# Kernel tuning notes

Hardware: AMD Instinct MI355X
Metric: run time of the kernel (lower is better)

## Reference

```python
import jax, jax.numpy as jnp
import numpy as np

INV_SQRT_4PI = 0.28209479177387814  # 1/sqrt(4*pi)

def sh_l(r, l):
    """Real spherical harmonics of unit vectors r [..., 3], e3nn order,
    'integral' normalization (e3nn o3.spherical_harmonics default)."""
    x, y, z = r[..., 0], r[..., 1], r[..., 2]
    if l == 0:
        return jnp.full(r.shape[:-1] + (1,), INV_SQRT_4PI, r.dtype)
    if l == 1:
        return 0.4886025119029199 * r  # sqrt(3/(4pi)) * (x, y, z)
    s15 = 3.872983346207417 * INV_SQRT_4PI   # sqrt(15)/sqrt(4pi)
    s5 = 2.23606797749979 * INV_SQRT_4PI     # sqrt(5)/sqrt(4pi)
    return jnp.stack([
        s15 * x * z,
        s15 * x * y,
        s5 * (y * y - 0.5 * (x * x + z * z)),
        s15 * y * z,
        0.5 * s15 * (z * z - x * x),
    ], axis=-1)

def layer_norm(x, g, b, eps=1e-5):
    mu = jnp.mean(x, axis=-1, keepdims=True)
    var = jnp.mean((x - mu) ** 2, axis=-1, keepdims=True)
    return (x - mu) * jax.lax.rsqrt(var + eps) * g + b

def setup_inputs() -> dict:
    key = jax.random.key(0)
    N, C, L = 1024, 128, 3  # nodes, sphere_channels, lmax+1
    ks = jax.random.split(key, 12)
    s = 0.02
    return {
        "x_emb": jax.random.normal(ks[0], (N, 9, C), jnp.float32),
        "pos": jax.random.normal(ks[1], (N, 3), jnp.float32) * 3.0,
        "q_w": jax.random.normal(ks[2], (C, C), jnp.float32) * s,
        "q_b": jnp.zeros((C,), jnp.float32),
        "k_w": jax.random.normal(ks[3], (C, C), jnp.float32) * s,
        "k_b": jnp.zeros((C,), jnp.float32),
        "v_w": jax.random.normal(ks[4], (L, C, C), jnp.float32) * s,
        "v_b0": jnp.zeros((C,), jnp.float32),
        "out_w": jax.random.normal(ks[5], (L, C, C), jnp.float32) * s,
        "ln_g": jnp.ones((L, C), jnp.float32),
        "ln_b": jnp.zeros((L, C), jnp.float32),
        "batch": jnp.sort(jax.random.randint(ks[6], (N,), 0, 16)).astype(jnp.int64),
    }

def reference(x_emb, pos, q_w, q_b, k_w, k_b, v_w, v_b0, out_w, ln_g, ln_b, batch):
    N, _, C = x_emb.shape
    H = 8
    D = C // H
    degs = (1, 3, 5)  # 2l+1 for l = 0, 1, 2

    # pairwise unit displacements  [N, N, 3]
    diff = pos[:, None, :] - pos[None, :, :]
    dist = jnp.maximum(jnp.linalg.norm(diff, axis=-1, keepdims=True), 1e-8)
    r_hat = diff / dist

    same = batch[:, None] == batch[None, :]           # [N, N]
    valid = same & ~jnp.eye(N, dtype=bool)

    # per-degree features: split x_emb[:, 9, C] into [1, 3, 5]
    feats = [x_emb[:, 0:1], x_emb[:, 1:4], x_emb[:, 4:9]]

    # HTR invariant pairwise score  [N, N, C]
    score = jnp.zeros((N, N, C), x_emb.dtype)
    for l, f in enumerate(feats):
        sh = sh_l(r_hat, l)                           # [N, N, 2l+1]
        score = score + jnp.einsum('imc,ijm->ijc', f, sh) / degs[l]
    score = score * valid[..., None].astype(score.dtype)

    q = (score.mean(axis=1) @ q_w.T + q_b).reshape(N, H, D)
    k = (score.mean(axis=0) @ k_w.T + k_b).reshape(N, H, D)

    attn = jnp.einsum('ihd,jhd->hij', q, k) * (D ** -0.5)
    attn = jnp.where(same[None], attn, -jnp.inf)
    attn = jnp.nan_to_num(jax.nn.softmax(attn, axis=-1))

    outs = []
    for l, f in enumerate(feats):
        m = degs[l]
        v = f @ v_w[l].T
        if l == 0:
            v = v + v_b0
        v = v.reshape(N, m, H, D)
        o = jnp.einsum('hij,jmhd->imhd', attn, v).reshape(N, m, C)
        o = o @ out_w[l].T
        outs.append(layer_norm(f + o, ln_g[l], ln_b[l]))
    return jnp.concatenate(outs, axis=1)
```

## Files before the change

kernel.cpp:

```cpp
#include <hip/hip_runtime.h>
#include <hip/hip_bf16.h>
#include <math.h>

#define NN 1024

typedef __attribute__((ext_vector_type(8))) short bf16x8;
typedef __attribute__((ext_vector_type(4))) float f32x4;

__device__ __forceinline__ float wave_sum(float v) {
#pragma unroll
  for (int off = 32; off > 0; off >>= 1) v += __shfl_down(v, off);
  return v;
}
__device__ __forceinline__ float wave_max(float v) {
#pragma unroll
  for (int off = 32; off > 0; off >>= 1) v = fmaxf(v, __shfl_down(v, off));
  return v;
}
__device__ __forceinline__ short f2bf(float x) {
  __hip_bfloat16 b = __float2bfloat16(x);
  return *(short*)&b;
}

#define SH_C0 0.28209479177387814f
#define SH_C1 0.4886025119029199f
#define SH_S15 1.0925484305920792f
#define SH_S5 0.6307831305050401f

__global__ __launch_bounds__(256) void htr_geom(
    const float* __restrict__ qw, const float* __restrict__ kw,
    const float* __restrict__ vw, const float* __restrict__ ow,
    const float* __restrict__ x_emb, const float* __restrict__ pos,
    const int* __restrict__ batch, const float* __restrict__ k_b,
    short* __restrict__ wbf, short* __restrict__ x_bf,
    short* __restrict__ fkT, short* __restrict__ Wsh,
    short* __restrict__ rowm_bf, float* __restrict__ khbuf) {
  const int b = blockIdx.x;
  const int tid = threadIdx.x;
  __shared__ short tile[128][36];
  __shared__ float red[4][9];
  __shared__ float sm[9];

  if (b < 8) {
    const float* src;
    if (b == 0) src = qw;
    else if (b == 1) src = kw;
    else if (b < 5) src = vw + (b - 2) * 16384;
    else src = ow + (b - 5) * 16384;
    short* dst = wbf + b * 16384;
    for (int idx = tid; idx < 16384; idx += 256) dst[idx] = f2bf(src[idx]);
  } else if (b < 1160) {
    int base = (b - 8) * 1024 + tid * 4;
    float4 v = *(const float4*)(x_emb + base);
    *(short4*)(x_bf + base) = make_short4(f2bf(v.x), f2bf(v.y), f2bf(v.z), f2bf(v.w));
  } else if (b < 1448) {
    const int sub = b - 1160;
    const int i0 = (sub & 31) * 32;
    const int m = sub >> 5;
    const int w = tid >> 6, lane = tid & 63;
    const int q = lane >> 4, l15 = lane & 15;
    const int isub = (w & 1) * 16;
    const int cbase = (w >> 1) * 64;
    bf16x8 a[4];
#pragma unroll
    for (int ks = 0; ks < 4; ++ks) {
      const float* ap = x_emb + ((i0 + isub + l15) * 9 + m) * 128 + ks * 32 + q * 8;
      bf16x8 av;
#pragma unroll
      for (int e = 0; e < 8; ++e) av[e] = f2bf(ap[e]);
      a[ks] = av;
    }
#pragma unroll
    for (int t = 0; t < 4; ++t) {
      f32x4 acc = (f32x4){0.f, 0.f, 0.f, 0.f};
#pragma unroll
      for (int ks = 0; ks < 4; ++ks) {
        const float* bp = kw + (cbase + t * 16 + l15) * 128 + ks * 32 + q * 8;
        bf16x8 bv;
#pragma unroll
        for (int e = 0; e < 8; ++e) bv[e] = f2bf(bp[e]);
        acc = __builtin_amdgcn_mfma_f32_16x16x32_bf16(a[ks], bv, acc, 0, 0, 0);
      }
#pragma unroll
      for (int r = 0; r < 4; ++r)
        tile[cbase + t * 16 + l15][isub + q * 4 + r] = f2bf(acc[r]);
    }
    __syncthreads();
    const int cc = tid >> 1, seg = tid & 1;
    short* dst = fkT + cc * 9216 + m * 1024 + i0 + seg * 16;
#pragma unroll
    for (int e = 0; e < 16; e += 2)
      *(short2*)(dst + e) = *(const short2*)(&tile[cc][seg * 16 + e]);
  } else if (b < 2472) {
    const int j = b - 1448;
    const float pjx = pos[j * 3 + 0], pjy = pos[j * 3 + 1], pjz = pos[j * 3 + 2];
    const int bj = batch[j];
    short* wrow = Wsh + j * 9216;
    for (int i = tid; i < 1024; i += 256) {
      float dx = pos[i * 3 + 0] - pjx;
      float dy = pos[i * 3 + 1] - pjy;
      float dz = pos[i * 3 + 2] - pjz;
      bool ok = (i != j) && (batch[i] == bj);
      float okf = ok ? 1.f : 0.f;
      float d2 = dx * dx + dy * dy + dz * dz;
      float inv = okf / fmaxf(sqrtf(d2), 1e-8f);
      float x = dx * inv, y = dy * inv, z = dz * inv;
      wrow[0 * 1024 + i] = f2bf(SH_C0 * okf);
      wrow[1 * 1024 + i] = f2bf((SH_C1 * (1.f / 3.f)) * x);
      wrow[2 * 1024 + i] = f2bf((SH_C1 * (1.f / 3.f)) * y);
      wrow[3 * 1024 + i] = f2bf((SH_C1 * (1.f / 3.f)) * z);
      wrow[4 * 1024 + i] = f2bf((SH_S15 * 0.2f) * x * z);
      wrow[5 * 1024 + i] = f2bf((SH_S15 * 0.2f) * x * y);
      wrow[6 * 1024 + i] = f2bf((SH_S5 * 0.2f) * (y * y - 0.5f * (x * x + z * z)));
      wrow[7 * 1024 + i] = f2bf((SH_S15 * 0.2f) * y * z);
      wrow[8 * 1024 + i] = f2bf((0.5f * SH_S15 * 0.2f) * (z * z - x * x));
    }
  } else if (b < 3496) {
    const int i = b - 2472;
    const float px = pos[i * 3 + 0], py = pos[i * 3 + 1], pz = pos[i * 3 + 2];
    const int bi = batch[i];
    float s[9];
#pragma unroll
    for (int m = 0; m < 9; ++m) s[m] = 0.f;
    for (int j = tid; j < NN; j += 256) {
      if (j == i) continue;
      if (batch[j] != bi) continue;
      float dx = px - pos[j * 3 + 0];
      float dy = py - pos[j * 3 + 1];
      float dz = pz - pos[j * 3 + 2];
      float d2 = dx * dx + dy * dy + dz * dz;
      float inv = 1.0f / fmaxf(sqrtf(d2), 1e-8f);
      float x = dx * inv, y = dy * inv, z = dz * inv;
      s[0] += 1.0f;
      s[1] += x; s[2] += y; s[3] += z;
      s[4] += x * z; s[5] += x * y;
      s[6] += y * y - 0.5f * (x * x + z * z);
      s[7] += y * z;
      s[8] += z * z - x * x;
    }
    const int wave = tid >> 6, lane = tid & 63;
#pragma unroll
    for (int m = 0; m < 9; ++m) {
      float v = wave_sum(s[m]);
      if (lane == 0) red[wave][m] = v;
    }
    __syncthreads();
    if (tid < 9) {
      float v = red[0][tid] + red[1][tid] + red[2][tid] + red[3][tid];
      float scl = SH_S15 * 0.2f;
      if (tid == 0) scl = SH_C0;
      else if (tid < 4) scl = SH_C1 * (1.f / 3.f);
      else if (tid == 6) scl = SH_S5 * 0.2f;
      else if (tid == 8) scl = 0.5f * SH_S15 * 0.2f;
      sm[tid] = v * scl * (1.0f / 1024.0f);
    }
    __syncthreads();
    if (tid < 128) {
      float acc = 0.f;
#pragma unroll
      for (int m = 0; m < 9; ++m)
        acc = fmaf(sm[m], x_emb[(i * 9 + m) * 128 + tid], acc);
      rowm_bf[i * 128 + tid] = f2bf(acc);
    }
  } else {
    const int base = (b - 3496) * 32768;
    for (int u = tid; u < 32768; u += 256) {
      const int idx = base + u;
      khbuf[idx] = k_b[((idx >> 14) << 4) | (idx & 15)];
    }
  }
}

__global__ __launch_bounds__(256) void htr_mid(
    const short* __restrict__ Wsh, const short* __restrict__ fkT,
    const short* __restrict__ rowm_bf, const short* __restrict__ x_bf,
    const short* __restrict__ wbf, const float* __restrict__ q_b,
    const float* __restrict__ v_b0, float* __restrict__ khbuf,
    float* __restrict__ qbuf, short* __restrict__ vbT) {
  const int b = blockIdx.x;
  const int tid = threadIdx.x;
  const int w = tid >> 6, lane = tid & 63;
  const int q = lane >> 4, l15 = lane & 15;
  __shared__ short bt[32][584];

  if (b < 256) {
    const int jb = (b & 15) * 64;
    const int ks = b >> 4;
    const int j = jb + w * 16 + l15;
    const short* ap = Wsh + j * 9216 + ks * 576 + q * 8;
    bf16x8 A[18];
#pragma unroll
    for (int s = 0; s < 18; ++s) A[s] = *(const bf16x8*)(ap + s * 32);

    f32x4 acc[8];
#pragma unroll
    for (int t = 0; t < 8; ++t) acc[t] = (f32x4){0.f, 0.f, 0.f, 0.f};

    for (int tc = 0; tc < 4; ++tc) {
      __syncthreads();
#pragma unroll
      for (int it = 0; it < 9; ++it) {
        int idx = tid + it * 256;
        int c = idx / 72;
        int g = idx - c * 72;
        *(bf16x8*)(&bt[c][g * 8]) =
            *(const bf16x8*)(fkT + (tc * 32 + c) * 9216 + ks * 576 + g * 8);
      }
      __syncthreads();
#pragma unroll
      for (int tl = 0; tl < 2; ++tl) {
        const int t = tc * 2 + tl;
        const short* brow = &bt[tl * 16 + l15][q * 8];
#pragma unroll
        for (int s = 0; s < 18; ++s) {
          bf16x8 bv = *(const bf16x8*)(brow + s * 32);
          acc[t] = __builtin_amdgcn_mfma_f32_16x16x32_bf16(A[s], bv, acc[t], 0, 0, 0);
        }
      }
    }
#pragma unroll
    for (int t = 0; t < 8; ++t)
#pragma unroll
      for (int r = 0; r < 4; ++r)
        atomicAdd(&khbuf[(t * 1024 + jb + w * 16 + q * 4 + r) * 16 + l15],
                  acc[t][r] * (1.0f / 1024.0f));
  } else if (b < 272) {
    const int ibase = ((b - 256) * 4 + w) * 16;
    const short* ap = rowm_bf + (ibase + l15) * 128 + q * 8;
    const short* bp = wbf + l15 * 128 + q * 8;
    bf16x8 a[4];
#pragma unroll
    for (int ks = 0; ks < 4; ++ks) a[ks] = *(const bf16x8*)(ap + ks * 32);
    f32x4 acc[8];
#pragma unroll
    for (int t = 0; t < 8; ++t) {
      acc[t] = (f32x4){0.f, 0.f, 0.f, 0.f};
      const short* btp = bp + t * 2048;
#pragma unroll
      for (int ks = 0; ks < 4; ++ks) {
        bf16x8 bv = *(const bf16x8*)(btp + ks * 32);
        acc[t] = __builtin_amdgcn_mfma_f32_16x16x32_bf16(a[ks], bv, acc[t], 0, 0, 0);
      }
    }
#pragma unroll
    for (int t = 0; t < 8; ++t) {
      float bo = q_b[t * 16 + l15];
#pragma unroll
      for (int r = 0; r < 4; ++r)
        qbuf[(ibase + q * 4 + r) * 128 + t * 16 + l15] = acc[t][r] + bo;
    }
  } else {
    const int u = (b - 272) * 4 + w;
    const int m = u >> 6;
    const int ibase = (u & 63) * 16;
    const int l = (m == 0) ? 0 : ((m < 4) ? 1 : 2);
    const short* ap = x_bf + ((ibase + l15) * 9 + m) * 128 + q * 8;
    const short* bp = wbf + (2 + l) * 16384 + l15 * 128 + q * 8;
    bf16x8 a[4];
#pragma unroll
    for (int ks = 0; ks < 4; ++ks) a[ks] = *(const bf16x8*)(ap + ks * 32);
    f32x4 acc[8];
#pragma unroll
    for (int t = 0; t < 8; ++t) {
      acc[t] = (f32x4){0.f, 0.f, 0.f, 0.f};
      const short* btp = bp + t * 2048;
#pragma unroll
      for (int ks = 0; ks < 4; ++ks) {
        bf16x8 bv = *(const bf16x8*)(btp + ks * 32);
        acc[t] = __builtin_amdgcn_mfma_f32_16x16x32_bf16(a[ks], bv, acc[t], 0, 0, 0);
      }
    }
#pragma unroll
    for (int t = 0; t < 8; ++t) {
      float bias = (m == 0) ? v_b0[t * 16 + l15] : 0.f;
#pragma unroll
      for (int r = 0; r < 4; ++r)
        vbT[(t * 144 + m * 16 + l15) * 1024 + ibase + q * 4 + r] =
            f2bf(acc[t][r] + bias);
    }
  }
}

template <int NT0, int NT>
__device__ __forceinline__ void apply_phase(
    const short* P, const short* __restrict__ vbT,
    short* __restrict__ obuf_bf, int ibase, int h, int lane) {
  const int q = lane >> 4, l15 = lane & 15;
  const int xs = (l15 & 7) << 3;
  const short* pr = P + l15 * 1024;
  const short* bp = vbT + (h * 144 + l15) * 1024 + q * 8;
  f32x4 acc[NT];
#pragma unroll
  for (int t = 0; t < NT; ++t) acc[t] = (f32x4){0.f, 0.f, 0.f, 0.f};
  bf16x8 a = *(const bf16x8*)(pr + ((q * 8) ^ xs));
  bf16x8 b[NT];
#pragma unroll
  for (int t = 0; t < NT; ++t) b[t] = *(const bf16x8*)(bp + (NT0 + t) * 16384);
  for (int ks = 1; ks < 32; ++ks) {
    const int off = ks * 32;
    bf16x8 an = *(const bf16x8*)(pr + ((off + q * 8) ^ xs));
    bf16x8 bn[NT];
#pragma unroll
    for (int t = 0; t < NT; ++t)
      bn[t] = *(const bf16x8*)(bp + (NT0 + t) * 16384 + off);
#pragma unroll
    for (int t = 0; t < NT; ++t)
      acc[t] = __builtin_amdgcn_mfma_f32_16x16x32_bf16(a, b[t], acc[t], 0, 0, 0);
    a = an;
#pragma unroll
    for (int t = 0; t < NT; ++t) b[t] = bn[t];
  }
#pragma unroll
  for (int t = 0; t < NT; ++t)
    acc[t] = __builtin_amdgcn_mfma_f32_16x16x32_bf16(a, b[t], acc[t], 0, 0, 0);
#pragma unroll
  for (int t = 0; t < NT; ++t)
#pragma unroll
    for (int r = 0; r < 4; ++r)
      obuf_bf[((ibase + q * 4 + r) * 9 + NT0 + t) * 128 + h * 16 + l15] =
          f2bf(acc[t][r]);
}

__global__ __launch_bounds__(256) void htr_attn_apply(
    const float* __restrict__ qbuf, const float* __restrict__ khbuf,
    const int* __restrict__ batch, const short* __restrict__ vbT,
    short* __restrict__ obuf_bf) {
  const int ibase = blockIdx.x * 16;
  const int h = blockIdx.y;
  const int tid = threadIdx.x;
  const int w = tid >> 6;
  const int lane = tid & 63;
  __shared__ short P[16 * 1024];

  const int r0 = ibase + w * 4;
  float qr[4][16];
  int bi[4];
#pragma unroll
  for (int r = 0; r < 4; ++r) {
    bi[r] = batch[r0 + r];
    const float* qp = qbuf + (r0 + r) * 128 + h * 16;
#pragma unroll
    for (int d = 0; d < 16; ++d) qr[r][d] = qp[d] * 0.25f;
  }
  float s[4][16];
#pragma unroll
  for (int jt = 0; jt < 16; ++jt) {
    const int j = jt * 64 + lane;
    const int bj = batch[j];
    const float4* kp = (const float4*)(khbuf + (h * 1024 + j) * 16);
    float4 k0 = kp[0], k1 = kp[1], k2 = kp[2], k3 = kp[3];
#pragma unroll
    for (int r = 0; r < 4; ++r) {
      float d = 0.f;
      d = fmaf(qr[r][0], k0.x, d);  d = fmaf(qr[r][1], k0.y, d);
      d = fmaf(qr[r][2], k0.z, d);  d = fmaf(qr[r][3], k0.w, d);
      d = fmaf(qr[r][4], k1.x, d);  d = fmaf(qr[r][5], k1.y, d);
      d = fmaf(qr[r][6], k1.z, d);  d = fmaf(qr[r][7], k1.w, d);
      d = fmaf(qr[r][8], k2.x, d);  d = fmaf(qr[r][9], k2.y, d);
      d = fmaf(qr[r][10], k2.z, d); d = fmaf(qr[r][11], k2.w, d);
      d = fmaf(qr[r][12], k3.x, d); d = fmaf(qr[r][13], k3.y, d);
      d = fmaf(qr[r][14], k3.z, d); d = fmaf(qr[r][15], k3.w, d);
      s[r][jt] = (bj == bi[r]) ? d : -INFINITY;
    }
  }
#pragma unroll
  for (int r = 0; r < 4; ++r) {
    float mx = s[r][0];
#pragma unroll
    for (int jt = 1; jt < 16; ++jt) mx = fmaxf(mx, s[r][jt]);
    mx = wave_max(mx);
    mx = __shfl(mx, 0);
    float t = 0.f;
#pragma unroll
    for (int jt = 0; jt < 16; ++jt) {
      s[r][jt] = expf(s[r][jt] - mx);
      t += s[r][jt];
    }
    t = wave_sum(t);
    t = __shfl(t, 0);
    const float inv = 1.0f / t;
    const int row = w * 4 + r;
    const int xs = (row & 7) << 3;
    short* pw = P + row * 1024;
#pragma unroll
    for (int jt = 0; jt < 16; ++jt) {
      const int j = jt * 64 + lane;
      pw[j ^ xs] = f2bf(s[r][jt] * inv);
    }
  }
  __syncthreads();

  if (w == 0)      apply_phase<0, 3>(P, vbT, obuf_bf, ibase, h, lane);
  else if (w == 1) apply_phase<3, 2>(P, vbT, obuf_bf, ibase, h, lane);
  else if (w == 2) apply_phase<5, 2>(P, vbT, obuf_bf, ibase, h, lane);
  else             apply_phase<7, 2>(P, vbT, obuf_bf, ibase, h, lane);
}

__global__ __launch_bounds__(64) void htr_outln_mfma(
    const short* __restrict__ obuf_bf, const float* __restrict__ x_emb,
    const short* __restrict__ wbf, const float* __restrict__ ln_g,
    const float* __restrict__ ln_b, float* __restrict__ out) {
  const int ibase = blockIdx.x * 16;
  const int m = blockIdx.y;
  const int l = (m == 0) ? 0 : ((m < 4) ? 1 : 2);
  const int lane = threadIdx.x;
  const int q = lane >> 4, l15 = lane & 15;
  const short* ap = obuf_bf + ((ibase + l15) * 9 + m) * 128 + q * 8;
  const short* bp = wbf + (5 + l) * 16384 + l15 * 128 + q * 8;
  bf16x8 a[4];
#pragma unroll
  for (int ks = 0; ks < 4; ++ks) a[ks] = *(const bf16x8*)(ap + ks * 32);
  f32x4 acc[8];
#pragma unroll
  for (int t = 0; t < 8; ++t) {
    acc[t] = (f32x4){0.f, 0.f, 0.f, 0.f};
    const short* bt = bp + t * 2048;
#pragma unroll
    for (int ks = 0; ks < 4; ++ks) {
      bf16x8 b = *(const bf16x8*)(bt + ks * 32);
      acc[t] = __builtin_amdgcn_mfma_f32_16x16x32_bf16(a[ks], b, acc[t], 0, 0, 0);
    }
  }
  float g[8], bb[8];
#pragma unroll
  for (int t = 0; t < 8; ++t) {
    g[t] = ln_g[l * 128 + t * 16 + l15];
    bb[t] = ln_b[l * 128 + t * 16 + l15];
  }
#pragma unroll
  for (int r = 0; r < 4; ++r) {
    const int i = ibase + q * 4 + r;
    const float* xr = x_emb + (i * 9 + m) * 128;
    float v[8];
    float sv = 0.f, sq = 0.f;
#pragma unroll
    for (int t = 0; t < 8; ++t) {
      v[t] = acc[t][r] + xr[t * 16 + l15];
      sv += v[t];
      sq += v[t] * v[t];
    }
#pragma unroll
    for (int off = 1; off < 16; off <<= 1) {
      sv += __shfl_xor(sv, off);
      sq += __shfl_xor(sq, off);
    }
    float mu = sv * (1.f / 128.f);
    float var = sq * (1.f / 128.f) - mu * mu;
    float rs = rsqrtf(var + 1e-5f);
    float* orow = out + (i * 9 + m) * 128;
#pragma unroll
    for (int t = 0; t < 8; ++t)
      orow[t * 16 + l15] = (v[t] - mu) * rs * g[t] + bb[t];
  }
}

extern "C" void kernel_launch(void* const* d_in, const int* in_sizes, int n_in,
                              void* d_out, int out_size, void* d_ws, size_t ws_size,
                              hipStream_t stream) {
  (void)in_sizes; (void)n_in; (void)out_size; (void)ws_size;
  const float* x_emb = (const float*)d_in[0];
  const float* pos   = (const float*)d_in[1];
  const float* q_w   = (const float*)d_in[2];
  const float* q_b   = (const float*)d_in[3];
  const float* k_w   = (const float*)d_in[4];
  const float* k_b   = (const float*)d_in[5];
  const float* v_w   = (const float*)d_in[6];
  const float* v_b0  = (const float*)d_in[7];
  const float* out_w = (const float*)d_in[8];
  const float* ln_g  = (const float*)d_in[9];
  const float* ln_b  = (const float*)d_in[10];
  const int*   batch = (const int*)d_in[11];
  float* out = (float*)d_out;

  float* ws = (float*)d_ws;
  short* rowm_bf = (short*)(ws + 0);
  float* qbuf    = ws + 65536;
  float* khbuf   = ws + 196608;
  short* wbf     = (short*)(ws + 327680);
  short* x_bf    = (short*)(ws + 393216);
  short* vbT     = (short*)(ws + 983040);
  short* obuf_bf = (short*)(ws + 1572864);
  short* Wsh     = (short*)(ws + 6356992);
  short* fkT     = (short*)(ws + 11075584);

  htr_geom<<<3500, 256, 0, stream>>>(q_w, k_w, v_w, out_w, x_emb, pos, batch,
                                     k_b, wbf, x_bf, fkT, Wsh, rowm_bf, khbuf);
  htr_mid<<<416, 256, 0, stream>>>(Wsh, fkT, rowm_bf, x_bf, wbf, q_b, v_b0,
                                   khbuf, qbuf, vbT);
  htr_attn_apply<<<dim3(64, 8), 256, 0, stream>>>(qbuf, khbuf, batch, vbT,
                                                  obuf_bf);
  htr_outln_mfma<<<dim3(64, 9), 64, 0, stream>>>(obuf_bf, x_emb, wbf, ln_g,
                                                 ln_b, out);
}
```

Measured before the change: 152.6 us.

## Compute spherical-harmonic weights in registers inside mid GEMM instead of materializing Wsh

Removes the geometry pass that wrote a 1024x9216 bf16 spherical-harmonic matrix to global memory. The mid kernel now loads positions and batch ids for a 64x64 node tile into shared memory and builds its MFMA A-fragments directly in registers. The fkT loads are re-indexed so the reduction is split by i-block rather than the old k-slice layout. This avoids about 19 MB of global writes and reads in exchange for recomputing square roots and divides inside the GEMM blocks.

```diff
diff --git a/kernel.cpp b/kernel.cpp
--- a/kernel.cpp
+++ b/kernel.cpp
@@ -33,8 +33,8 @@
     const float* __restrict__ x_emb, const float* __restrict__ pos,
     const int* __restrict__ batch, const float* __restrict__ k_b,
     short* __restrict__ wbf, short* __restrict__ x_bf,
-    short* __restrict__ fkT, short* __restrict__ Wsh,
-    short* __restrict__ rowm_bf, float* __restrict__ khbuf) {
+    short* __restrict__ fkT, short* __restrict__ rowm_bf,
+    float* __restrict__ khbuf) {
   const int b = blockIdx.x;
   const int tid = threadIdx.x;
   __shared__ short tile[128][36];
@@ -92,31 +92,7 @@
     for (int e = 0; e < 16; e += 2)
       *(short2*)(dst + e) = *(const short2*)(&tile[cc][seg * 16 + e]);
   } else if (b < 2472) {
-    const int j = b - 1448;
-    const float pjx = pos[j * 3 + 0], pjy = pos[j * 3 + 1], pjz = pos[j * 3 + 2];
-    const int bj = batch[j];
-    short* wrow = Wsh + j * 9216;
-    for (int i = tid; i < 1024; i += 256) {
-      float dx = pos[i * 3 + 0] - pjx;
-      float dy = pos[i * 3 + 1] - pjy;
-      float dz = pos[i * 3 + 2] - pjz;
-      bool ok = (i != j) && (batch[i] == bj);
-      float okf = ok ? 1.f : 0.f;
-      float d2 = dx * dx + dy * dy + dz * dz;
-      float inv = okf / fmaxf(sqrtf(d2), 1e-8f);
-      float x = dx * inv, y = dy * inv, z = dz * inv;
-      wrow[0 * 1024 + i] = f2bf(SH_C0 * okf);
-      wrow[1 * 1024 + i] = f2bf((SH_C1 * (1.f / 3.f)) * x);
-      wrow[2 * 1024 + i] = f2bf((SH_C1 * (1.f / 3.f)) * y);
-      wrow[3 * 1024 + i] = f2bf((SH_C1 * (1.f / 3.f)) * z);
-      wrow[4 * 1024 + i] = f2bf((SH_S15 * 0.2f) * x * z);
-      wrow[5 * 1024 + i] = f2bf((SH_S15 * 0.2f) * x * y);
-      wrow[6 * 1024 + i] = f2bf((SH_S5 * 0.2f) * (y * y - 0.5f * (x * x + z * z)));
-      wrow[7 * 1024 + i] = f2bf((SH_S15 * 0.2f) * y * z);
-      wrow[8 * 1024 + i] = f2bf((0.5f * SH_S15 * 0.2f) * (z * z - x * x));
-    }
-  } else if (b < 3496) {
-    const int i = b - 2472;
+    const int i = b - 1448;
     const float px = pos[i * 3 + 0], py = pos[i * 3 + 1], pz = pos[i * 3 + 2];
     const int bi = batch[i];
     float s[9];
@@ -163,7 +139,7 @@
       rowm_bf[i * 128 + tid] = f2bf(acc);
     }
   } else {
-    const int base = (b - 3496) * 32768;
+    const int base = (b - 2472) * 32768;
     for (int u = tid; u < 32768; u += 256) {
       const int idx = base + u;
       khbuf[idx] = k_b[((idx >> 14) << 4) | (idx & 15)];
@@ -172,25 +148,72 @@
 }
 
 __global__ __launch_bounds__(256) void htr_mid(
-    const short* __restrict__ Wsh, const short* __restrict__ fkT,
-    const short* __restrict__ rowm_bf, const short* __restrict__ x_bf,
-    const short* __restrict__ wbf, const float* __restrict__ q_b,
-    const float* __restrict__ v_b0, float* __restrict__ khbuf,
-    float* __restrict__ qbuf, short* __restrict__ vbT) {
+    const float* __restrict__ pos, const int* __restrict__ batch,
+    const short* __restrict__ fkT, const short* __restrict__ rowm_bf,
+    const short* __restrict__ x_bf, const short* __restrict__ wbf,
+    const float* __restrict__ q_b, const float* __restrict__ v_b0,
+    float* __restrict__ khbuf, float* __restrict__ qbuf,
+    short* __restrict__ vbT) {
   const int b = blockIdx.x;
   const int tid = threadIdx.x;
   const int w = tid >> 6, lane = tid & 63;
   const int q = lane >> 4, l15 = lane & 15;
   __shared__ short bt[32][584];
+  __shared__ float4 pj_s[64], pi_s[64];
 
   if (b < 256) {
     const int jb = (b & 15) * 64;
-    const int ks = b >> 4;
-    const int j = jb + w * 16 + l15;
-    const short* ap = Wsh + j * 9216 + ks * 576 + q * 8;
+    const int ib = (b >> 4) * 64;
+    if (tid < 64)
+      pj_s[tid] = make_float4(pos[(jb + tid) * 3 + 0], pos[(jb + tid) * 3 + 1],
+                              pos[(jb + tid) * 3 + 2],
+                              __int_as_float(batch[jb + tid]));
+    else if (tid < 128) {
+      const int u = tid - 64;
+      pi_s[u] = make_float4(pos[(ib + u) * 3 + 0], pos[(ib + u) * 3 + 1],
+                            pos[(ib + u) * 3 + 2],
+                            __int_as_float(batch[ib + u]));
+    }
+    __syncthreads();
+
+    const int jl = w * 16 + l15;
+    const int j = jb + jl;
+    const float4 pj = pj_s[jl];
+    const int bj = __float_as_int(pj.w);
+
     bf16x8 A[18];
-#pragma unroll
-    for (int s = 0; s < 18; ++s) A[s] = *(const bf16x8*)(ap + s * 32);
+    {
+#pragma unroll
+      for (int half = 0; half < 2; ++half) {
+        float gx[8], gy[8], gz[8], go[8];
+#pragma unroll
+        for (int e = 0; e < 8; ++e) {
+          const int il = half * 32 + q * 8 + e;
+          const float4 pi = pi_s[il];
+          const bool ok = ((ib + il) != j) && (__float_as_int(pi.w) == bj);
+          const float okf = ok ? 1.f : 0.f;
+          const float dx = pi.x - pj.x;
+          const float dy = pi.y - pj.y;
+          const float dz = pi.z - pj.z;
+          const float d2 = dx * dx + dy * dy + dz * dz;
+          const float inv = okf / fmaxf(sqrtf(d2), 1e-8f);
+          gx[e] = dx * inv; gy[e] = dy * inv; gz[e] = dz * inv; go[e] = okf;
+        }
+#pragma unroll
+        for (int e = 0; e < 8; ++e) {
+          const float x = gx[e], y = gy[e], z = gz[e], okf = go[e];
+          A[0 + half][e] = f2bf(SH_C0 * okf);
+          A[2 + half][e] = f2bf((SH_C1 * (1.f / 3.f)) * x);
+          A[4 + half][e] = f2bf((SH_C1 * (1.f / 3.f)) * y);
+          A[6 + half][e] = f2bf((SH_C1 * (1.f / 3.f)) * z);
+          A[8 + half][e] = f2bf((SH_S15 * 0.2f) * x * z);
+          A[10 + half][e] = f2bf((SH_S15 * 0.2f) * x * y);
+          A[12 + half][e] = f2bf((SH_S5 * 0.2f) * (y * y - 0.5f * (x * x + z * z)));
+          A[14 + half][e] = f2bf((SH_S15 * 0.2f) * y * z);
+          A[16 + half][e] = f2bf((0.5f * SH_S15 * 0.2f) * (z * z - x * x));
+        }
+      }
+    }
 
     f32x4 acc[8];
 #pragma unroll
@@ -204,7 +227,8 @@
         int c = idx / 72;
         int g = idx - c * 72;
         *(bf16x8*)(&bt[c][g * 8]) =
-            *(const bf16x8*)(fkT + (tc * 32 + c) * 9216 + ks * 576 + g * 8);
+            *(const bf16x8*)(fkT + (tc * 32 + c) * 9216 + (g >> 3) * 1024 + ib +
+                             (g & 7) * 8);
       }
       __syncthreads();
 #pragma unroll
@@ -480,13 +504,12 @@
   short* x_bf    = (short*)(ws + 393216);
   short* vbT     = (short*)(ws + 983040);
   short* obuf_bf = (short*)(ws + 1572864);
-  short* Wsh     = (short*)(ws + 6356992);
   short* fkT     = (short*)(ws + 11075584);
 
-  htr_geom<<<3500, 256, 0, stream>>>(q_w, k_w, v_w, out_w, x_emb, pos, batch,
-                                     k_b, wbf, x_bf, fkT, Wsh, rowm_bf, khbuf);
-  htr_mid<<<416, 256, 0, stream>>>(Wsh, fkT, rowm_bf, x_bf, wbf, q_b, v_b0,
-                                   khbuf, qbuf, vbT);
+  htr_geom<<<2476, 256, 0, stream>>>(q_w, k_w, v_w, out_w, x_emb, pos, batch,
+                                     k_b, wbf, x_bf, fkT, rowm_bf, khbuf);
+  htr_mid<<<416, 256, 0, stream>>>(pos, batch, fkT, rowm_bf, x_bf, wbf, q_b,
+                                   v_b0, khbuf, qbuf, vbT);
   htr_attn_apply<<<dim3(64, 8), 256, 0, stream>>>(qbuf, khbuf, batch, vbT,
                                                   obuf_bf);
   htr_outln_mfma<<<dim3(64, 9), 64, 0, stream>>>(obuf_bf, x_emb, wbf, ln_g,
```

New measurement: 151.6 us. About the same (-0.7%).
